# Kernel tuning notes

Hardware: AMD Instinct MI355X
Metric: run time of the kernel (lower is better)

## Reference

```python
import jax, jax.numpy as jnp
import numpy as np

N_NODES = 10000
N_EDGES = 320000
N_GRAPHS = 64


def _seg_max0(data, seg, num_segments):
    # segment max; empty segments get 0 (matches PyG scatter-max fill behavior)
    agg = jax.ops.segment_max(data, seg, num_segments=num_segments)
    return jnp.where(jnp.isneginf(agg), 0.0, agg)


def _edge_conv(x, src, dst, W, b, n_nodes):
    # PyG EdgeConv: message = nn(cat([x_i, x_j - x_i])), aggr='max' at target i
    xi = x[dst]                       # [E, d]
    xj = x[src]                       # [E, d]
    m = jax.nn.sigmoid(jnp.concatenate([xi, xj - xi], axis=-1) @ W + b)  # [E, d_out]
    return _seg_max0(m, dst, n_nodes)


def setup_inputs() -> dict:
    key = jax.random.key(0)
    ks = jax.random.split(key, 12)
    x = jax.random.normal(ks[0], (N_NODES, 3), dtype=jnp.float32)
    edge_index = jax.random.randint(ks[1], (2, N_EDGES), 0, N_NODES, dtype=jnp.int64)
    batch = jnp.sort(jax.random.randint(ks[2], (N_NODES,), 0, N_GRAPHS, dtype=jnp.int64))

    def lin(k, fan_in, fan_out):
        kw, kb = jax.random.split(k)
        lim = 1.0 / np.sqrt(fan_in)
        W = jax.random.uniform(kw, (fan_in, fan_out), jnp.float32, -lim, lim)
        b = jax.random.uniform(kb, (fan_out,), jnp.float32, -lim, lim)
        return W, b

    W1, b1 = lin(ks[3], 6, 128)     # EdgeConv1 MLP: Linear(2*3, 128)
    W2, b2 = lin(ks[4], 256, 256)   # EdgeConv2 MLP: Linear(2*128, 256)
    W3, b3 = lin(ks[5], 256, 128)   # output Linear(256, 128)
    W4, b4 = lin(ks[6], 128, 10)    # output Linear(128, output_classes)
    return {"x": x, "edge_index": edge_index, "batch": batch,
            "W1": W1, "b1": b1, "W2": W2, "b2": b2,
            "W3": W3, "b3": b3, "W4": W4, "b4": b4}


def reference(x, edge_index, batch, W1, b1, W2, b2, W3, b3, W4, b4):
    src, dst = edge_index[0], edge_index[1]
    h = _edge_conv(x, src, dst, W1, b1, N_NODES)    # [N, 128]
    h = _edge_conv(h, src, dst, W2, b2, N_NODES)    # [N, 256]
    g = _seg_max0(h, batch, N_GRAPHS)               # [G, 256] graph max-pool
    out = jax.nn.sigmoid(g @ W3 + b3) @ W4 + b4     # [G, 10]
    return out
```

## Files before the change

kernel.cpp:

```cpp
#include <hip/hip_runtime.h>

#define N_NODES  10000
#define N_EDGES  320000
#define N_GRAPHS 64
#define STRIDE   192

#define RB 1250
#define RQ 157
#define RW 256

typedef __attribute__((ext_vector_type(8))) __bf16 bf16x8;
typedef __attribute__((ext_vector_type(4))) float f32x4;
typedef __attribute__((ext_vector_type(4))) unsigned int u32x4;

__device__ __forceinline__ float sigm(float z) { return 1.0f / (1.0f + __expf(-z)); }

__device__ __forceinline__ unsigned short f2bf(float f) {
    unsigned int u = __float_as_uint(f);
    return (unsigned short)((u + 0x7fffu + ((u >> 16) & 1u)) >> 16);
}
__device__ __forceinline__ float bf2f(unsigned short h) { return __uint_as_float(((unsigned int)h) << 16); }
__device__ __forceinline__ float bflo(unsigned int u) { return __uint_as_float(u << 16); }
__device__ __forceinline__ float bfhi(unsigned int u) { return __uint_as_float(u & 0xffff0000u); }

__global__ __launch_bounds__(256) void prep_k(
        const unsigned int* __restrict__ ei_raw, const unsigned int* __restrict__ b_raw,
        const float* __restrict__ x, const float* __restrict__ W1,
        const float* __restrict__ W2,
        int* __restrict__ bat, int* __restrict__ cnt, unsigned short* __restrict__ csr_pad,
        unsigned short* __restrict__ Q1,
        unsigned short* __restrict__ Bh, unsigned short* __restrict__ Bl,
        float* __restrict__ g) {
    int bx = blockIdx.x, t = threadIdx.x;
    if (bx < RB) {
        __shared__ int snz[2];
        if (t < 2) snz[t] = 0;
        __syncthreads();
        {
            unsigned int wv = ei_raw[bx * 512 + 2 * t + 1];
            unsigned long long m = __ballot(wv != 0);
            if ((t & 63) == 0 && m) atomicAdd(&snz[0], __popcll(m));
        }
        if (bx * 256 < N_NODES) {
            int w0 = min(bx * 512, N_NODES - 512);
            unsigned int bv = b_raw[w0 + 2 * t + 1];
            unsigned long long m = __ballot(bv != 0);
            if ((t & 63) == 0 && m) atomicAdd(&snz[1], __popcll(m));
        }
        __syncthreads();
        int i = bx * 256 + t;
        int i32e = snz[0] > 16;
        const int* ei = (const int*)ei_raw;
        if (i < N_EDGES) {
            int s = i32e ? ei[i] : ei[2 * i];
            int d = i32e ? ei[N_EDGES + i] : ei[2 * (N_EDGES + i)];
            int slot = atomicAdd(&cnt[d], 1);
            if (slot < STRIDE) csr_pad[d * STRIDE + slot] = (unsigned short)s;
        }
        if (i < N_NODES) {
            int i32b = snz[1] > 16;
            const int* bb = (const int*)b_raw;
            bat[i] = i32b ? bb[i] : bb[2 * i];
        }
    } else if (bx < RB + RQ) {
        __shared__ float xs[192];
        int c = t & 127, half = t >> 7;
        float k0 = W1[384 + c];
        float k1 = W1[512 + c];
        float k2 = W1[640 + c];
        int n0 = (bx - RB) * 64;
        int nmax = min(64, N_NODES - n0);
        if (t < 192) xs[t] = (t < nmax * 3) ? x[n0 * 3 + t] : 0.f;
        __syncthreads();
        for (int tt = 0; tt < 32; tt++) {
            int ln = 2 * tt + half;
            if (ln < nmax) {
                float v = xs[ln * 3 + 0] * k0 + xs[ln * 3 + 1] * k1 + xs[ln * 3 + 2] * k2;
                Q1[(n0 + ln) * 128 + c] = f2bf(v);
            }
        }
    } else if (bx < RB + RQ + RW) {
        int idx = (bx - RB - RQ) * 256 + t;
        int nn = idx >> 7, k = idx & 127;
        float wc;
        if (nn < 256) wc = W2[k * 256 + nn] - W2[(128 + k) * 256 + nn];
        else          wc = W2[(128 + k) * 256 + (nn - 256)];
        unsigned short h = f2bf(wc);
        Bh[idx] = h;
        Bl[idx] = f2bf(wc - bf2f(h));
    } else {
        float4 z = make_float4(0.f, 0.f, 0.f, 0.f);
#pragma unroll
        for (int it = 0; it < 16; it++) *(float4*)&g[(t + it * 256) * 4] = z;
    }
}

__global__ __launch_bounds__(256) void econv1_k(
        const float* __restrict__ x, const float* __restrict__ W1, const float* __restrict__ b1,
        const unsigned int* __restrict__ Q1u,
        const int* __restrict__ cnt, const unsigned short* __restrict__ csr_pad,
        unsigned short* __restrict__ h1h, unsigned short* __restrict__ h1l) {
    int lane = threadIdx.x & 63;
    int i = blockIdx.x * 4 + (threadIdx.x >> 6);
    if (i >= N_NODES) return;
    int e = min(cnt[i], STRIDE);
    float o0 = 0.f, o1 = 0.f;
    if (e > 0) {
        const unsigned short* row = csr_pad + (size_t)i * STRIDE;
        float z0 = -3.4e38f, z1 = -3.4e38f;
        int last = e - 1;
        for (int k = 0; k < e; k += 16) {
            uint4 ra = *(const uint4*)&row[k];
            uint4 rb = *(const uint4*)&row[k + 8];
            unsigned int rw[8] = {ra.x, ra.y, ra.z, ra.w, rb.x, rb.y, rb.z, rb.w};
            int j0 = rw[0] & 0xffff;
            unsigned int u[16];
#pragma unroll
            for (int tt = 0; tt < 16; tt++) {
                int raw = (rw[tt >> 1] >> ((tt & 1) * 16)) & 0xffff;
                int j = (k + tt <= last) ? raw : j0;
                u[tt] = Q1u[j * 64 + lane];
            }
#pragma unroll
            for (int tt = 0; tt < 16; tt++) {
                z0 = fmaxf(z0, bflo(u[tt]));
                z1 = fmaxf(z1, bfhi(u[tt]));
            }
        }
        float x0 = x[i * 3 + 0], x1 = x[i * 3 + 1], x2 = x[i * 3 + 2];
        int c0 = 2 * lane, c1 = 2 * lane + 1;
        float p0 = b1[c0] + x0 * (W1[c0] - W1[384 + c0]) + x1 * (W1[128 + c0] - W1[512 + c0]) +
                   x2 * (W1[256 + c0] - W1[640 + c0]);
        float p1 = b1[c1] + x0 * (W1[c1] - W1[384 + c1]) + x1 * (W1[128 + c1] - W1[512 + c1]) +
                   x2 * (W1[256 + c1] - W1[640 + c1]);
        o0 = sigm(p0 + z0);
        o1 = sigm(p1 + z1);
    }
    unsigned short hh0 = f2bf(o0), hh1 = f2bf(o1);
    unsigned short hl0 = f2bf(o0 - bf2f(hh0)), hl1 = f2bf(o1 - bf2f(hh1));
    *(ushort2*)&h1h[i * 128 + 2 * lane] = make_ushort2(hh0, hh1);
    *(ushort2*)&h1l[i * 128 + 2 * lane] = make_ushort2(hl0, hl1);
}

__global__ __launch_bounds__(256) void gemm2_k(
        const unsigned short* __restrict__ Ahg, const unsigned short* __restrict__ Alg,
        const unsigned short* __restrict__ Bhg, const unsigned short* __restrict__ Blg,
        const float* __restrict__ b2, float* __restrict__ P2,
        unsigned short* __restrict__ Q2, int n) {
    __shared__ __align__(16) char smem[65536];
    char* Ahb = smem;
    char* Alb = smem + 16384;
    char* Bhb = smem + 32768;
    char* Blb = smem + 49152;
    int t = threadIdx.x;
    int m0 = blockIdx.x * 64;
    int n0 = blockIdx.y * 64;
#pragma unroll
    for (int it = 0; it < 4; it++) {
        int c = t + it * 256;
        int row = c >> 4, kb = c & 15;
        int dsa = (row * 256 + kb * 16) ^ ((row & 7) << 4);
        u32x4 va = {0u, 0u, 0u, 0u}, vl = {0u, 0u, 0u, 0u};
        if (m0 + row < n) {
            va = *(const u32x4*)&Ahg[(m0 + row) * 128 + kb * 8];
            vl = *(const u32x4*)&Alg[(m0 + row) * 128 + kb * 8];
        }
        *(u32x4*)(Ahb + dsa) = va;
        *(u32x4*)(Alb + dsa) = vl;
        *(u32x4*)(Bhb + dsa) = *(const u32x4*)&Bhg[(n0 + row) * 128 + kb * 8];
        *(u32x4*)(Blb + dsa) = *(const u32x4*)&Blg[(n0 + row) * 128 + kb * 8];
    }
    __syncthreads();

    int w = t >> 6, lane = t & 63;
    int lr = lane & 15, lg = lane >> 4;
    int am = 16 * w + lr;
    int abase = am * 256 + lg * 16;
    int asw = (am & 7) << 4;
    bf16x8 ah[4], al[4];
#pragma unroll
    for (int kk = 0; kk < 4; kk++) {
        int off = (abase + kk * 64) ^ asw;
        ah[kk] = *(const bf16x8*)(Ahb + off);
        al[kk] = *(const bf16x8*)(Alb + off);
    }
    int bsw = (lr & 7) << 4;
#pragma unroll
    for (int nt = 0; nt < 4; nt++) {
        int nb = (nt * 16 + lr) * 256 + lg * 16;
        f32x4 acc = {0.f, 0.f, 0.f, 0.f};
#pragma unroll
        for (int kk = 0; kk < 4; kk++) {
            int off = (nb + kk * 64) ^ bsw;
            bf16x8 bh = *(const bf16x8*)(Bhb + off);
            bf16x8 bl = *(const bf16x8*)(Blb + off);
            acc = __builtin_amdgcn_mfma_f32_16x16x32_bf16(ah[kk], bh, acc, 0, 0, 0);
            acc = __builtin_amdgcn_mfma_f32_16x16x32_bf16(al[kk], bh, acc, 0, 0, 0);
            acc = __builtin_amdgcn_mfma_f32_16x16x32_bf16(ah[kk], bl, acc, 0, 0, 0);
        }
        int colg = n0 + nt * 16 + lr;
        int mbase = m0 + 16 * w + 4 * lg;
        if (colg < 256) {
            float bias = b2[colg];
#pragma unroll
            for (int r = 0; r < 4; r++) {
                int m = mbase + r;
                if (m < n)
                    __builtin_nontemporal_store(acc[r] + bias, &P2[(size_t)m * 256 + colg]);
            }
        } else {
            int qc = colg - 256;
#pragma unroll
            for (int r = 0; r < 4; r++) {
                int m = mbase + r;
                if (m < n) Q2[(size_t)m * 256 + qc] = f2bf(acc[r]);
            }
        }
    }
}

__global__ __launch_bounds__(256) void econv2_k(
        const float* __restrict__ P2, const unsigned int* __restrict__ Q2u,
        const int* __restrict__ cnt, const unsigned short* __restrict__ csr_pad,
        const int* __restrict__ bat, float* __restrict__ g) {
    int lane = threadIdx.x & 63;
    int w = threadIdx.x >> 6;
    int i = blockIdx.x * 2 + (w >> 1);
    if (i >= N_NODES) return;
    int e = min(cnt[i], STRIDE);
    if (e == 0) return;
    int cc = (w & 1) * 64 + lane;
    const unsigned short* row = csr_pad + (size_t)i * STRIDE;
    float z0 = -3.4e38f, z1 = -3.4e38f;
    int last = e - 1;
    for (int k = 0; k < e; k += 16) {
        uint4 ra = *(const uint4*)&row[k];
        uint4 rb = *(const uint4*)&row[k + 8];
        unsigned int rw[8] = {ra.x, ra.y, ra.z, ra.w, rb.x, rb.y, rb.z, rb.w};
        int j0 = rw[0] & 0xffff;
        unsigned int u[16];
#pragma unroll
        for (int tt = 0; tt < 16; tt++) {
            int raw = (rw[tt >> 1] >> ((tt & 1) * 16)) & 0xffff;
            int j = (k + tt <= last) ? raw : j0;
            u[tt] = Q2u[j * 128 + cc];
        }
#pragma unroll
        for (int tt = 0; tt < 16; tt++) {
            z0 = fmaxf(z0, bflo(u[tt]));
            z1 = fmaxf(z1, bfhi(u[tt]));
        }
    }
    unsigned long long pv =
        __builtin_nontemporal_load((const unsigned long long*)&P2[(size_t)i * 256 + 2 * cc]);
    float px = __uint_as_float((unsigned int)pv);
    float py = __uint_as_float((unsigned int)(pv >> 32));
    int gb = bat[i] * 256 + 2 * cc;
    atomicMax((unsigned int*)&g[gb + 0], __float_as_uint(sigm(px + z0)));
    atomicMax((unsigned int*)&g[gb + 1], __float_as_uint(sigm(py + z1)));
}

__global__ void final_k(const float* __restrict__ g, const float* __restrict__ W3,
                        const float* __restrict__ b3, const float* __restrict__ W4,
                        const float* __restrict__ b4, float* __restrict__ out) {
    __shared__ float gs[256];
    __shared__ float ss[128];
    int b = blockIdx.x, t = threadIdx.x;
    gs[t] = g[b * 256 + t];
    gs[t + 128] = g[b * 256 + 128 + t];
    __syncthreads();
    float acc = b3[t];
#pragma unroll 8
    for (int k = 0; k < 256; k++) acc += gs[k] * W3[k * 128 + t];
    ss[t] = sigm(acc);
    __syncthreads();
    if (t < 10) {
        float o = b4[t];
#pragma unroll 8
        for (int k = 0; k < 128; k++) o += ss[k] * W4[k * 10 + t];
        out[b * 10 + t] = o;
    }
}

extern "C" void kernel_launch(void* const* d_in, const int* in_sizes, int n_in,
                              void* d_out, int out_size, void* d_ws, size_t ws_size,
                              hipStream_t stream) {
    const float* x  = (const float*)d_in[0];
    const void*  ei_raw = d_in[1];
    const void*  b_raw  = d_in[2];
    const float* W1 = (const float*)d_in[3];
    const float* b1 = (const float*)d_in[4];
    const float* W2 = (const float*)d_in[5];
    const float* b2 = (const float*)d_in[6];
    const float* W3 = (const float*)d_in[7];
    const float* b3 = (const float*)d_in[8];
    const float* W4 = (const float*)d_in[9];
    const float* b4 = (const float*)d_in[10];

    char* ws = (char*)d_ws;
    size_t off = 0;
    auto alloc = [&](size_t bytes) {
        void* p = ws + off;
        off += (bytes + 255) & ~(size_t)255;
        return p;
    };
    int*            bat     = (int*)alloc(N_NODES * 4);
    int*            cnt     = (int*)alloc(N_NODES * 4);
    unsigned short* csr_pad = (unsigned short*)alloc((size_t)N_NODES * STRIDE * 2);
    unsigned short* Q1      = (unsigned short*)alloc((size_t)N_NODES * 128 * 2);
    unsigned short* h1h     = (unsigned short*)alloc((size_t)N_NODES * 128 * 2);
    unsigned short* h1l     = (unsigned short*)alloc((size_t)N_NODES * 128 * 2);
    unsigned short* Bh      = (unsigned short*)alloc(512 * 128 * 2);
    unsigned short* Bl      = (unsigned short*)alloc(512 * 128 * 2);
    float*          P2      = (float*)alloc((size_t)N_NODES * 256 * 4);
    unsigned short* Q2      = (unsigned short*)alloc((size_t)N_NODES * 256 * 2);
    float*          g       = (float*)alloc(N_GRAPHS * 256 * 4);

    hipMemsetAsync(cnt, 0, N_NODES * 4, stream);

    prep_k<<<RB + RQ + RW + 1, 256, 0, stream>>>(
        (const unsigned int*)ei_raw, (const unsigned int*)b_raw, x, W1, W2,
        bat, cnt, csr_pad, Q1, Bh, Bl, g);

    econv1_k<<<(N_NODES + 3) / 4, 256, 0, stream>>>(x, W1, b1, (const unsigned int*)Q1,
                                                    cnt, csr_pad, h1h, h1l);
    gemm2_k<<<dim3((N_NODES + 63) / 64, 8), 256, 0, stream>>>(h1h, h1l, Bh, Bl, b2, P2, Q2, N_NODES);

    econv2_k<<<(N_NODES + 1) / 2, 256, 0, stream>>>(P2, (const unsigned int*)Q2,
                                                    cnt, csr_pad, bat, g);
    final_k<<<N_GRAPHS, 128, 0, stream>>>(g, W3, b3, W4, b4, (float*)d_out);
}
```

Before: 179.2 us.

## Process two edges per thread in CSR build and hoist loads before gathers

The CSR build now handles two edges per thread with vectorized index loads, which halves the number of edge blocks. econv1 and econv2 hoist their per-node parameter, P2 and batch loads ahead of the neighbor gather loop so that latency can overlap. Bounds checks are dropped because N_NODES divides evenly by the block counts. The nontemporal store and load hints on P2 are replaced with ordinary accesses so P2 can stay in cache between gemm2 and econv2.

New measurement: 176.1 us. About the same (-1.7%).

```diff
diff --git a/kernel.cpp b/kernel.cpp
--- a/kernel.cpp
+++ b/kernel.cpp
@@ -5,7 +5,7 @@
 #define N_GRAPHS 64
 #define STRIDE   192
 
-#define RB 1250
+#define RB 625
 #define RQ 157
 #define RW 256
 
@@ -37,7 +37,7 @@
         if (t < 2) snz[t] = 0;
         __syncthreads();
         {
-            unsigned int wv = ei_raw[bx * 512 + 2 * t + 1];
+            unsigned int wv = ei_raw[bx * 1024 + 2 * t + 1];
             unsigned long long m = __ballot(wv != 0);
             if ((t & 63) == 0 && m) atomicAdd(&snz[0], __popcll(m));
         }
@@ -48,15 +48,24 @@
             if ((t & 63) == 0 && m) atomicAdd(&snz[1], __popcll(m));
         }
         __syncthreads();
-        int i = bx * 256 + t;
         int i32e = snz[0] > 16;
         const int* ei = (const int*)ei_raw;
-        if (i < N_EDGES) {
-            int s = i32e ? ei[i] : ei[2 * i];
-            int d = i32e ? ei[N_EDGES + i] : ei[2 * (N_EDGES + i)];
-            int slot = atomicAdd(&cnt[d], 1);
-            if (slot < STRIDE) csr_pad[d * STRIDE + slot] = (unsigned short)s;
-        }
+        int e0 = bx * 512 + 2 * t;
+        int s0, s1, d0, d1;
+        if (i32e) {
+            uint2 sv = *(const uint2*)&ei[e0];
+            uint2 dv = *(const uint2*)&ei[N_EDGES + e0];
+            s0 = sv.x; s1 = sv.y; d0 = dv.x; d1 = dv.y;
+        } else {
+            uint4 sv = *(const uint4*)&ei[2 * e0];
+            uint4 dv = *(const uint4*)&ei[2 * (N_EDGES + e0)];
+            s0 = sv.x; s1 = sv.z; d0 = dv.x; d1 = dv.z;
+        }
+        int slot = atomicAdd(&cnt[d0], 1);
+        if (slot < STRIDE) csr_pad[d0 * STRIDE + slot] = (unsigned short)s0;
+        slot = atomicAdd(&cnt[d1], 1);
+        if (slot < STRIDE) csr_pad[d1 * STRIDE + slot] = (unsigned short)s1;
+        int i = bx * 256 + t;
         if (i < N_NODES) {
             int i32b = snz[1] > 16;
             const int* bb = (const int*)b_raw;
@@ -102,8 +111,16 @@
         unsigned short* __restrict__ h1h, unsigned short* __restrict__ h1l) {
     int lane = threadIdx.x & 63;
     int i = blockIdx.x * 4 + (threadIdx.x >> 6);
-    if (i >= N_NODES) return;
     int e = min(cnt[i], STRIDE);
+    int c0 = 2 * lane, c1 = c0 + 1;
+    float x0 = x[i * 3 + 0], x1 = x[i * 3 + 1], x2 = x[i * 3 + 2];
+    float bb0 = b1[c0], bb1 = b1[c1];
+    float wa0 = W1[c0] - W1[384 + c0];
+    float wb0 = W1[128 + c0] - W1[512 + c0];
+    float wc0 = W1[256 + c0] - W1[640 + c0];
+    float wa1 = W1[c1] - W1[384 + c1];
+    float wb1 = W1[128 + c1] - W1[512 + c1];
+    float wc1 = W1[256 + c1] - W1[640 + c1];
     float o0 = 0.f, o1 = 0.f;
     if (e > 0) {
         const unsigned short* row = csr_pad + (size_t)i * STRIDE;
@@ -127,12 +144,8 @@
                 z1 = fmaxf(z1, bfhi(u[tt]));
             }
         }
-        float x0 = x[i * 3 + 0], x1 = x[i * 3 + 1], x2 = x[i * 3 + 2];
-        int c0 = 2 * lane, c1 = 2 * lane + 1;
-        float p0 = b1[c0] + x0 * (W1[c0] - W1[384 + c0]) + x1 * (W1[128 + c0] - W1[512 + c0]) +
-                   x2 * (W1[256 + c0] - W1[640 + c0]);
-        float p1 = b1[c1] + x0 * (W1[c1] - W1[384 + c1]) + x1 * (W1[128 + c1] - W1[512 + c1]) +
-                   x2 * (W1[256 + c1] - W1[640 + c1]);
+        float p0 = bb0 + x0 * wa0 + x1 * wb0 + x2 * wc0;
+        float p1 = bb1 + x0 * wa1 + x1 * wb1 + x2 * wc1;
         o0 = sigm(p0 + z0);
         o1 = sigm(p1 + z1);
     }
@@ -205,8 +218,7 @@
 #pragma unroll
             for (int r = 0; r < 4; r++) {
                 int m = mbase + r;
-                if (m < n)
-                    __builtin_nontemporal_store(acc[r] + bias, &P2[(size_t)m * 256 + colg]);
+                if (m < n) P2[(size_t)m * 256 + colg] = acc[r] + bias;
             }
         } else {
             int qc = colg - 256;
@@ -226,10 +238,11 @@
     int lane = threadIdx.x & 63;
     int w = threadIdx.x >> 6;
     int i = blockIdx.x * 2 + (w >> 1);
-    if (i >= N_NODES) return;
     int e = min(cnt[i], STRIDE);
     if (e == 0) return;
     int cc = (w & 1) * 64 + lane;
+    unsigned long long pv = *(const unsigned long long*)&P2[(size_t)i * 256 + 2 * cc];
+    int gb = bat[i] * 256 + 2 * cc;
     const unsigned short* row = csr_pad + (size_t)i * STRIDE;
     float z0 = -3.4e38f, z1 = -3.4e38f;
     int last = e - 1;
@@ -251,11 +264,8 @@
             z1 = fmaxf(z1, bfhi(u[tt]));
         }
     }
-    unsigned long long pv =
-        __builtin_nontemporal_load((const unsigned long long*)&P2[(size_t)i * 256 + 2 * cc]);
     float px = __uint_as_float((unsigned int)pv);
     float py = __uint_as_float((unsigned int)(pv >> 32));
-    int gb = bat[i] * 256 + 2 * cc;
     atomicMax((unsigned int*)&g[gb + 0], __float_as_uint(sigm(px + z0)));
     atomicMax((unsigned int*)&g[gb + 1], __float_as_uint(sigm(py + z1)));
 }
@@ -322,11 +332,11 @@
         (const unsigned int*)ei_raw, (const unsigned int*)b_raw, x, W1, W2,
         bat, cnt, csr_pad, Q1, Bh, Bl, g);
 
-    econv1_k<<<(N_NODES + 3) / 4, 256, 0, stream>>>(x, W1, b1, (const unsigned int*)Q1,
-                                                    cnt, csr_pad, h1h, h1l);
+    econv1_k<<<N_NODES / 4, 256, 0, stream>>>(x, W1, b1, (const unsigned int*)Q1,
+                                              cnt, csr_pad, h1h, h1l);
     gemm2_k<<<dim3((N_NODES + 63) / 64, 8), 256, 0, stream>>>(h1h, h1l, Bh, Bl, b2, P2, Q2, N_NODES);
 
-    econv2_k<<<(N_NODES + 1) / 2, 256, 0, stream>>>(P2, (const unsigned int*)Q2,
-                                                    cnt, csr_pad, bat, g);
+    econv2_k<<<N_NODES / 2, 256, 0, stream>>>(P2, (const unsigned int*)Q2,
+                                              cnt, csr_pad, bat, g);
     final_k<<<N_GRAPHS, 128, 0, stream>>>(g, W3, b3, W4, b4, (float*)d_out);
 }
```
